# Kernel tuning notes

Hardware: AMD Instinct MI355X
Metric: run time of the kernel (lower is better)

## Reference

```python
import jax, jax.numpy as jnp
import numpy as np

EMBED = 1024
HEADS = 16
HEAD_DIM = EMBED // HEADS


def setup_inputs() -> dict:
    key = jax.random.key(0)
    ks = jax.random.split(key, 6)
    N, S, E = 2, 2048, EMBED
    value = jax.random.normal(ks[0], (N, S, E), dtype=jnp.float32)
    k = jax.random.normal(ks[1], (N, S, E), dtype=jnp.float32)
    q = jax.random.normal(ks[2], (N, S, E), dtype=jnp.float32)
    mask = jax.random.randint(ks[3], (N, 1, S, S), 0, 2, dtype=jnp.int32)
    W_fc = jax.random.normal(ks[4], (E, E), dtype=jnp.float32) * (1.0 / np.sqrt(E))
    b_fc = jax.random.normal(ks[5], (E,), dtype=jnp.float32) * 0.01
    return {"value": value, "key": k, "query": q, "mask": mask, "W_fc": W_fc, "b_fc": b_fc}


def reference(value, key, query, mask, W_fc, b_fc):
    N, Sq, E = query.shape
    Sk = key.shape[1]
    Sv = value.shape[1]
    # NOTE: the original module never applies its q/k/v Linear layers (source bug);
    # it only reshapes into heads.
    v = value.reshape(N, Sv, HEADS, HEAD_DIM)
    k = key.reshape(N, Sk, HEADS, HEAD_DIM)
    q = query.reshape(N, Sq, HEADS, HEAD_DIM)
    # energy: [N, H, Q, K]
    energy = jnp.einsum('nqhd,nkhd->nhqk', q, k)
    energy = jnp.where(mask == 0, jnp.float32(-1e20), energy)
    # scale by sqrt(embed_size) as in the source (not sqrt(head_dim))
    attention = jax.nn.softmax(energy / jnp.sqrt(jnp.float32(E)), axis=3)
    out = jnp.einsum('nhql,nlhd->nqhd', attention, v).reshape(N, Sq, E)
    # torch Linear: x @ W.T + b
    out = out @ W_fc.T + b_fc
    return out
```

## Files before the change

kernel.cpp:

```cpp
#include <hip/hip_runtime.h>
#include <hip/hip_bf16.h>
#include <math.h>

#define S_LEN 2048
#define EMB   1024
#define HEADS 16
#define HDIM  64
#define SPLIT 2
#define NITER ((S_LEN / SPLIT) / 64)

#define C_SCALE   0.045084439f
#define BIAS_OK  -2.0f

#define NE  ((size_t)2 * S_LEN * EMB)
#define NL  ((size_t)2 * S_LEN * HEADS)
#define NMB ((size_t)2 * S_LEN * S_LEN / 64)
#define NTILE_ELEMS 4096

typedef __bf16 bf16x8 __attribute__((ext_vector_type(8)));
typedef float  f32x4  __attribute__((ext_vector_type(4)));
typedef float  f32x16 __attribute__((ext_vector_type(16)));

__device__ __forceinline__ bf16x8 cvt8(const float* v) {
    bf16x8 r;
#pragma unroll
    for (int i = 0; i < 8; ++i) r[i] = (__bf16)v[i];
    return r;
}
__device__ __forceinline__ unsigned long long pack4(float a, float b, float c, float d) {
    __bf16 t[4] = {(__bf16)a, (__bf16)b, (__bf16)c, (__bf16)d};
    return *(unsigned long long*)t;
}
__device__ __forceinline__ bf16x8 cat2(unsigned long long lo, unsigned long long hi) {
    unsigned long long t[2] = {lo, hi};
    return *(bf16x8*)t;
}
__device__ __forceinline__ void gld_lds16(const void* g, void* l) {
    __builtin_amdgcn_global_load_lds(
        (const __attribute__((address_space(1))) void*)g,
        (__attribute__((address_space(3))) void*)l, 16, 0, 0);
}

__global__ __launch_bounds__(256)
void prepass_kernel(const float* __restrict__ Kp, const float* __restrict__ Vp,
                    const float* __restrict__ Wf, const int* __restrict__ Mp,
                    __bf16* __restrict__ Kb, __bf16* __restrict__ Vtb,
                    __bf16* __restrict__ Wb, unsigned long long* __restrict__ Mb) {
    __shared__ __bf16 Lp[64 * 72];
    const int bid = blockIdx.x, tid = threadIdx.x;

    if (bid < 1024) {
        const int tile = bid;
        const int n = tile >> 9, h = (tile >> 5) & 15, kvt = tile & 31;
        const int r = tid >> 2, d0 = (tid & 3) * 16;
        const float* src = Kp + ((size_t)n * S_LEN + kvt * 64 + r) * EMB + h * 64 + d0;
        float t[16];
        *(float4*)&t[0]  = *(const float4*)src;
        *(float4*)&t[4]  = *(const float4*)(src + 4);
        *(float4*)&t[8]  = *(const float4*)(src + 8);
        *(float4*)&t[12] = *(const float4*)(src + 12);
        char* img = (char*)(Kb + (size_t)tile * NTILE_ELEMS);
        *(bf16x8*)(img + r * 128 + ((d0 * 2)       ^ ((r & 7) << 4))) = cvt8(&t[0]);
        *(bf16x8*)(img + r * 128 + (((d0 + 8) * 2) ^ ((r & 7) << 4))) = cvt8(&t[8]);
    } else if (bid < 2048) {
        const int tile = bid - 1024;
        const int n = tile >> 9, h = (tile >> 5) & 15, kvt = tile & 31;
        {
            const int kv = tid >> 2, d0 = (tid & 3) * 16;
            const float* src = Vp + ((size_t)n * S_LEN + kvt * 64 + kv) * EMB + h * 64 + d0;
            float t[16];
            *(float4*)&t[0]  = *(const float4*)src;
            *(float4*)&t[4]  = *(const float4*)(src + 4);
            *(float4*)&t[8]  = *(const float4*)(src + 8);
            *(float4*)&t[12] = *(const float4*)(src + 12);
            *(bf16x8*)&Lp[kv * 72 + d0]     = cvt8(&t[0]);
            *(bf16x8*)&Lp[kv * 72 + d0 + 8] = cvt8(&t[8]);
        }
        __syncthreads();
        {
            const int d = tid >> 2, kvg = (tid & 3) * 16;
            __bf16 a[16];
#pragma unroll
            for (int j = 0; j < 16; ++j) a[j] = Lp[(kvg + j) * 72 + d];
            char* img = (char*)(Vtb + (size_t)tile * NTILE_ELEMS);
            *(bf16x8*)(img + d * 128 + ((kvg * 2)        ^ ((d & 7) << 4))) = *(bf16x8*)&a[0];
            *(bf16x8*)(img + d * 128 + (((kvg + 16) * 2 - 16) ^ ((d & 7) << 4))) = *(bf16x8*)&a[8];
        }
    } else if (bid < 2560) {
        size_t i = (((size_t)(bid - 2048)) * 256 + tid) * 8;
        float t[8];
        *(float4*)&t[0] = *(const float4*)(Wf + i);
        *(float4*)&t[4] = *(const float4*)(Wf + i + 4);
        *(bf16x8*)(Wb + i) = cvt8(t);
    } else {
        const int w = tid >> 6, lane = tid & 63;
        const int wg = (bid - 2560) * 4 + w;
#pragma unroll 4
        for (int it = 0; it < 64; ++it) {
            size_t W = (size_t)wg * 64 + it;
            int v = Mp[W * 64 + lane];
            unsigned long long b = __ballot(v != 0);
            if (lane == 0) Mb[W] = b;
        }
    }
}

__global__ __launch_bounds__(256, 4)
void attn_kernel(const __bf16* __restrict__ Vtb, const __bf16* __restrict__ Kb,
                 const float* __restrict__ Qp, const unsigned long long* __restrict__ Mb,
                 __bf16* __restrict__ Opart, float* __restrict__ Lpart) {
    __shared__ __bf16 Klds[2][64 * 64];
    __shared__ __bf16 Vtlds[2][64 * 64];

    const int tid  = threadIdx.x;
    const int lane = tid & 63;
    const int w    = tid >> 6;
    const int nblk = 2 * HEADS * SPLIT * 16;
    const int bid  = (blockIdx.x & 7) * (nblk / 8) + (blockIdx.x >> 3);
    const int qt = bid & 15;
    const int sp = (bid >> 4) & (SPLIT - 1);
    const int h  = (bid >> 5) & 15;
    const int n  = bid >> 9;

    const int ql = lane & 31;
    const int g  = lane >> 5;

    const int q = qt * 128 + w * 32 + ql;

    bf16x8 qfrag[4];
#pragma unroll
    for (int ds_ = 0; ds_ < 4; ++ds_) {
        const float* qp = Qp + ((size_t)n * S_LEN + q) * EMB + h * HDIM + ds_ * 16 + g * 8;
        float tmp[8];
        *(float4*)&tmp[0] = *(const float4*)qp;
        *(float4*)&tmp[4] = *(const float4*)(qp + 4);
        qfrag[ds_] = cvt8(tmp);
    }

    f32x16 oacc[2] = {};
    f32x16 lacc = {};
    bf16x8 aon;
#pragma unroll
    for (int i = 0; i < 8; ++i) aon[i] = (__bf16)1.0f;

    const unsigned long long* mrow = Mb + ((size_t)(n * S_LEN + q) << 5) + sp * NITER;

    const __bf16* ktiles = Kb  + ((size_t)((n * 16 + h) * 32) + sp * NITER) * NTILE_ELEMS;
    const __bf16* vtiles = Vtb + ((size_t)((n * 16 + h) * 32) + sp * NITER) * NTILE_ELEMS;

#define STAGE(B, T) do {                                                              \
        const __bf16* kt_ = ktiles + (size_t)(T) * NTILE_ELEMS;                       \
        const __bf16* vt_ = vtiles + (size_t)(T) * NTILE_ELEMS;                       \
        __bf16* kl_ = Klds[B]  + w * 512;                                             \
        __bf16* vl_ = Vtlds[B] + w * 512;                                             \
        gld_lds16(kt_ + w * 512 + lane * 8,        kl_);                              \
        gld_lds16(kt_ + 2048 + w * 512 + lane * 8, kl_ + 2048);                       \
        gld_lds16(vt_ + w * 512 + lane * 8,        vl_);                              \
        gld_lds16(vt_ + 2048 + w * 512 + lane * 8, vl_ + 2048);                       \
    } while (0)

    STAGE(0, 0);
    __syncthreads();

#pragma unroll 1
    for (int t = 0; t < NITER; ++t) {
        const int buf = t & 1;
        if (t < NITER - 1) STAGE(buf ^ 1, t + 1);
        const unsigned long long m64 = mrow[t];

#pragma unroll
        for (int kt = 0; kt < 2; ++kt) {
            f32x16 E = {};
            __builtin_amdgcn_s_setprio(1);
#pragma unroll
            for (int ds_ = 0; ds_ < 4; ++ds_) {
                int row = kt * 32 + ql;
                bf16x8 kf = *(const bf16x8*)((char*)Klds[buf] + row * 128 +
                    ((ds_ * 32 + g * 16) ^ ((row & 7) << 4)));
                E = __builtin_amdgcn_mfma_f32_32x32x16_bf16(kf, qfrag[ds_], E, 0, 0, 0);
            }
            __builtin_amdgcn_s_setprio(0);

            const unsigned u = (unsigned)(m64 >> (kt * 32 + 4 * g));
            unsigned long long own[4];
#pragma unroll
            for (int rq = 0; rq < 4; ++rq) {
                unsigned nib = u >> (8 * rq);
                float p0 = __builtin_amdgcn_exp2f(fmaf(E[4*rq+0], C_SCALE, BIAS_OK)) * (float)(nib & 1u);
                float p1 = __builtin_amdgcn_exp2f(fmaf(E[4*rq+1], C_SCALE, BIAS_OK)) * (float)((nib >> 1) & 1u);
                float p2 = __builtin_amdgcn_exp2f(fmaf(E[4*rq+2], C_SCALE, BIAS_OK)) * (float)((nib >> 2) & 1u);
                float p3 = __builtin_amdgcn_exp2f(fmaf(E[4*rq+3], C_SCALE, BIAS_OK)) * (float)((nib >> 3) & 1u);
                own[rq] = pack4(p0, p1, p2, p3);
            }

            unsigned long long sa = g ? own[0] : own[1];
            unsigned long long sb = g ? own[2] : own[3];
            unsigned long long ra = __shfl_xor((long long)sa, 32);
            unsigned long long rb = __shfl_xor((long long)sb, 32);
            bf16x8 frag0 = g ? cat2(ra, own[1]) : cat2(own[0], ra);
            bf16x8 frag1 = g ? cat2(rb, own[3]) : cat2(own[2], rb);

            __builtin_amdgcn_s_setprio(1);
            lacc = __builtin_amdgcn_mfma_f32_32x32x16_bf16(aon, frag0, lacc, 0, 0, 0);
            lacc = __builtin_amdgcn_mfma_f32_32x32x16_bf16(aon, frag1, lacc, 0, 0, 0);
#pragma unroll
            for (int dt = 0; dt < 2; ++dt) {
                int row = dt * 32 + ql;
                bf16x8 v0 = *(const bf16x8*)((char*)Vtlds[buf] + row * 128 +
                    (((2*kt) * 32 + g * 16) ^ ((row & 7) << 4)));
                bf16x8 v1 = *(const bf16x8*)((char*)Vtlds[buf] + row * 128 +
                    (((2*kt+1) * 32 + g * 16) ^ ((row & 7) << 4)));
                oacc[dt] = __builtin_amdgcn_mfma_f32_32x32x16_bf16(v0, frag0, oacc[dt], 0, 0, 0);
                oacc[dt] = __builtin_amdgcn_mfma_f32_32x32x16_bf16(v1, frag1, oacc[dt], 0, 0, 0);
            }
            __builtin_amdgcn_s_setprio(0);
        }

        __syncthreads();
    }
#undef STAGE

    __bf16* op = Opart + (size_t)sp * NE + ((size_t)n * S_LEN + q) * EMB + h * HDIM;
#pragma unroll
    for (int dt = 0; dt < 2; ++dt)
#pragma unroll
        for (int rq = 0; rq < 4; ++rq)
            *(unsigned long long*)(op + dt * 32 + 8 * rq + 4 * g) =
                pack4(oacc[dt][4*rq], oacc[dt][4*rq+1], oacc[dt][4*rq+2], oacc[dt][4*rq+3]);
    if (g == 0)
        Lpart[(size_t)sp * NL + ((size_t)n * S_LEN + q) * HEADS + h] = lacc[0];
}

__global__ __launch_bounds__(256)
void reduce_kernel(const __bf16* __restrict__ Opart, const float* __restrict__ Lpart,
                   __bf16* __restrict__ X) {
    size_t e0 = ((size_t)blockIdx.x * 256 + threadIdx.x) * 8;
    size_t hr = e0 >> 6;
    float l = 0.f;
#pragma unroll
    for (int s = 0; s < SPLIT; ++s) l += Lpart[s * NL + hr];
    float inv = 1.f / l;
    float acc[8] = {};
#pragma unroll
    for (int s = 0; s < SPLIT; ++s) {
        bf16x8 v = *(const bf16x8*)(Opart + s * NE + e0);
#pragma unroll
        for (int i = 0; i < 8; ++i) acc[i] += (float)v[i];
    }
    bf16x8 r;
#pragma unroll
    for (int i = 0; i < 8; ++i) r[i] = (__bf16)(acc[i] * inv);
    *(bf16x8*)(X + e0) = r;
}

__global__ __launch_bounds__(256)
void fc_kernel(const __bf16* __restrict__ X, const __bf16* __restrict__ Wb,
               const float* __restrict__ bfc, float* __restrict__ Out) {
    __shared__ __bf16 Al[128 * 32];
    __shared__ __bf16 Bl[128 * 32];
    const int tid = threadIdx.x, lane = tid & 63, w = tid >> 6;
    const int ql = lane & 15, g = lane >> 4;
    const int bm = blockIdx.x >> 3, bn = blockIdx.x & 7;
    const int wr = w >> 1, wc = w & 1;

    const int rowL = lane >> 2;
    const int colE = (lane & 3) * 8;

    f32x4 acc[4][4] = {};

    for (int k0 = 0; k0 < EMB; k0 += 32) {
        __syncthreads();
        const int q0 = w * 2, q1 = w * 2 + 1;
        gld_lds16(X  + (size_t)(bm * 128 + q0 * 16 + rowL) * EMB + k0 + colE, Al + q0 * 512);
        gld_lds16(X  + (size_t)(bm * 128 + q1 * 16 + rowL) * EMB + k0 + colE, Al + q1 * 512);
        gld_lds16(Wb + (size_t)(bn * 128 + q0 * 16 + rowL) * EMB + k0 + colE, Bl + q0 * 512);
        gld_lds16(Wb + (size_t)(bn * 128 + q1 * 16 + rowL) * EMB + k0 + colE, Bl + q1 * 512);
        __syncthreads();

        bf16x8 a[4], b[4];
#pragma unroll
        for (int mi = 0; mi < 4; ++mi)
            a[mi] = *(const bf16x8*)(Al + (wr * 64 + mi * 16 + ql) * 32 + g * 8);
#pragma unroll
        for (int nj = 0; nj < 4; ++nj)
            b[nj] = *(const bf16x8*)(Bl + (wc * 64 + nj * 16 + ql) * 32 + g * 8);
#pragma unroll
        for (int mi = 0; mi < 4; ++mi)
#pragma unroll
            for (int nj = 0; nj < 4; ++nj)
                acc[mi][nj] = __builtin_amdgcn_mfma_f32_16x16x32_bf16(a[mi], b[nj], acc[mi][nj], 0, 0, 0);
    }

#pragma unroll
    for (int nj = 0; nj < 4; ++nj) {
        int col = bn * 128 + wc * 64 + nj * 16 + ql;
        float bias = bfc[col];
#pragma unroll
        for (int mi = 0; mi < 4; ++mi) {
            int row0 = bm * 128 + wr * 64 + mi * 16 + g * 4;
#pragma unroll
            for (int r = 0; r < 4; ++r)
                Out[(size_t)(row0 + r) * EMB + col] = acc[mi][nj][r] + bias;
        }
    }
}

extern "C" void kernel_launch(void* const* d_in, const int* in_sizes, int n_in,
                              void* d_out, int out_size, void* d_ws, size_t ws_size,
                              hipStream_t stream) {
    const float* Vp = (const float*)d_in[0];
    const float* Kp = (const float*)d_in[1];
    const float* Qp = (const float*)d_in[2];
    const int*   Mp = (const int*)d_in[3];
    const float* Wf = (const float*)d_in[4];
    const float* bf = (const float*)d_in[5];
    float* Out = (float*)d_out;

    char* p = (char*)d_ws;
    __bf16* Opart = (__bf16*)p;             p += SPLIT * NE * 2;
    float*  Lpart = (float*)p;              p += SPLIT * NL * 4;
    __bf16* Wb    = (__bf16*)p;             p += (size_t)EMB * EMB * 2;
    unsigned long long* Mb = (unsigned long long*)p; p += NMB * 8;
    __bf16* Kb    = (__bf16*)p;             p += (size_t)1024 * NTILE_ELEMS * 2;
    __bf16* Vtb   = (__bf16*)p;

    prepass_kernel<<<dim3(3072), dim3(256), 0, stream>>>(Kp, Vp, Wf, Mp, Kb, Vtb, Wb, Mb);
    attn_kernel<<<dim3(2 * HEADS * SPLIT * 16), dim3(256), 0, stream>>>(Vtb, Kb, Qp, Mb, Opart, Lpart);
    reduce_kernel<<<dim3(NE / 8 / 256), dim3(256), 0, stream>>>(Opart, Lpart, Opart);
    fc_kernel<<<dim3((2 * S_LEN / 128) * (EMB / 128)), dim3(256), 0, stream>>>(Opart, Wb, bf, Out);
}
```

Measured before the change: 126.7 us.

## Drop key-split in attention and fuse normalization, removing reduce kernel

```diff
diff --git a/kernel.cpp b/kernel.cpp
--- a/kernel.cpp
+++ b/kernel.cpp
@@ -6,14 +6,12 @@
 #define EMB   1024
 #define HEADS 16
 #define HDIM  64
-#define SPLIT 2
-#define NITER ((S_LEN / SPLIT) / 64)
+#define NITER 32
 
 #define C_SCALE   0.045084439f
 #define BIAS_OK  -2.0f
 
 #define NE  ((size_t)2 * S_LEN * EMB)
-#define NL  ((size_t)2 * S_LEN * HEADS)
 #define NMB ((size_t)2 * S_LEN * S_LEN / 64)
 #define NTILE_ELEMS 4096
 
@@ -108,19 +106,17 @@
 __global__ __launch_bounds__(256, 4)
 void attn_kernel(const __bf16* __restrict__ Vtb, const __bf16* __restrict__ Kb,
                  const float* __restrict__ Qp, const unsigned long long* __restrict__ Mb,
-                 __bf16* __restrict__ Opart, float* __restrict__ Lpart) {
+                 __bf16* __restrict__ X) {
     __shared__ __bf16 Klds[2][64 * 64];
     __shared__ __bf16 Vtlds[2][64 * 64];
 
     const int tid  = threadIdx.x;
     const int lane = tid & 63;
     const int w    = tid >> 6;
-    const int nblk = 2 * HEADS * SPLIT * 16;
-    const int bid  = (blockIdx.x & 7) * (nblk / 8) + (blockIdx.x >> 3);
+    const int bid  = (blockIdx.x & 7) * 64 + (blockIdx.x >> 3);
     const int qt = bid & 15;
-    const int sp = (bid >> 4) & (SPLIT - 1);
-    const int h  = (bid >> 5) & 15;
-    const int n  = bid >> 9;
+    const int h  = (bid >> 4) & 15;
+    const int n  = bid >> 8;
 
     const int ql = lane & 31;
     const int g  = lane >> 5;
@@ -143,10 +139,10 @@
 #pragma unroll
     for (int i = 0; i < 8; ++i) aon[i] = (__bf16)1.0f;
 
-    const unsigned long long* mrow = Mb + ((size_t)(n * S_LEN + q) << 5) + sp * NITER;
-
-    const __bf16* ktiles = Kb  + ((size_t)((n * 16 + h) * 32) + sp * NITER) * NTILE_ELEMS;
-    const __bf16* vtiles = Vtb + ((size_t)((n * 16 + h) * 32) + sp * NITER) * NTILE_ELEMS;
+    const unsigned long long* mrow = Mb + ((size_t)(n * S_LEN + q) << 5);
+
+    const __bf16* ktiles = Kb  + (size_t)((n * 16 + h) * 32) * NTILE_ELEMS;
+    const __bf16* vtiles = Vtb + (size_t)((n * 16 + h) * 32) * NTILE_ELEMS;
 
 #define STAGE(B, T) do {                                                              \
         const __bf16* kt_ = ktiles + (size_t)(T) * NTILE_ELEMS;                       \
@@ -220,37 +216,15 @@
     }
 #undef STAGE
 
-    __bf16* op = Opart + (size_t)sp * NE + ((size_t)n * S_LEN + q) * EMB + h * HDIM;
+    const float inv = 1.f / lacc[0];
+    __bf16* op = X + ((size_t)n * S_LEN + q) * EMB + h * HDIM;
 #pragma unroll
     for (int dt = 0; dt < 2; ++dt)
 #pragma unroll
         for (int rq = 0; rq < 4; ++rq)
             *(unsigned long long*)(op + dt * 32 + 8 * rq + 4 * g) =
-                pack4(oacc[dt][4*rq], oacc[dt][4*rq+1], oacc[dt][4*rq+2], oacc[dt][4*rq+3]);
-    if (g == 0)
-        Lpart[(size_t)sp * NL + ((size_t)n * S_LEN + q) * HEADS + h] = lacc[0];
-}
-
-__global__ __launch_bounds__(256)
-void reduce_kernel(const __bf16* __restrict__ Opart, const float* __restrict__ Lpart,
-                   __bf16* __restrict__ X) {
-    size_t e0 = ((size_t)blockIdx.x * 256 + threadIdx.x) * 8;
-    size_t hr = e0 >> 6;
-    float l = 0.f;
-#pragma unroll
-    for (int s = 0; s < SPLIT; ++s) l += Lpart[s * NL + hr];
-    float inv = 1.f / l;
-    float acc[8] = {};
-#pragma unroll
-    for (int s = 0; s < SPLIT; ++s) {
-        bf16x8 v = *(const bf16x8*)(Opart + s * NE + e0);
-#pragma unroll
-        for (int i = 0; i < 8; ++i) acc[i] += (float)v[i];
-    }
-    bf16x8 r;
-#pragma unroll
-    for (int i = 0; i < 8; ++i) r[i] = (__bf16)(acc[i] * inv);
-    *(bf16x8*)(X + e0) = r;
+                pack4(oacc[dt][4*rq] * inv, oacc[dt][4*rq+1] * inv,
+                      oacc[dt][4*rq+2] * inv, oacc[dt][4*rq+3] * inv);
 }
 
 __global__ __launch_bounds__(256)
@@ -317,15 +291,13 @@
     float* Out = (float*)d_out;
 
     char* p = (char*)d_ws;
-    __bf16* Opart = (__bf16*)p;             p += SPLIT * NE * 2;
-    float*  Lpart = (float*)p;              p += SPLIT * NL * 4;
-    __bf16* Wb    = (__bf16*)p;             p += (size_t)EMB * EMB * 2;
+    __bf16* X  = (__bf16*)p;                p += NE * 2;
+    __bf16* Wb = (__bf16*)p;                p += (size_t)EMB * EMB * 2;
     unsigned long long* Mb = (unsigned long long*)p; p += NMB * 8;
-    __bf16* Kb    = (__bf16*)p;             p += (size_t)1024 * NTILE_ELEMS * 2;
-    __bf16* Vtb   = (__bf16*)p;
+    __bf16* Kb  = (__bf16*)p;               p += (size_t)1024 * NTILE_ELEMS * 2;
+    __bf16* Vtb = (__bf16*)p;
 
     prepass_kernel<<<dim3(3072), dim3(256), 0, stream>>>(Kp, Vp, Wf, Mp, Kb, Vtb, Wb, Mb);
-    attn_kernel<<<dim3(2 * HEADS * SPLIT * 16), dim3(256), 0, stream>>>(Vtb, Kb, Qp, Mb, Opart, Lpart);
-    reduce_kernel<<<dim3(NE / 8 / 256), dim3(256), 0, stream>>>(Opart, Lpart, Opart);
-    fc_kernel<<<dim3((2 * S_LEN / 128) * (EMB / 128)), dim3(256), 0, stream>>>(Opart, Wb, bf, Out);
-}
+    attn_kernel<<<dim3(2 * HEADS * 16), dim3(256), 0, stream>>>(Vtb, Kb, Qp, Mb, X);
+    fc_kernel<<<dim3((2 * S_LEN / 128) * (EMB / 128)), dim3(256), 0, stream>>>(X, Wb, bf, Out);
+}
```

Result: no change. 127.8 us (+0.9%).
